# Optimization experiments

Measured on AMD Instinct MI355X. Metric: run time of the kernel, lower is better.

Reference implementation:

```python
import jax, jax.numpy as jnp
import numpy as np

NUM_HEADS = 8
NUM_LEVELS = 4
NUM_POINTS = 4


def setup_inputs() -> dict:
    key = jax.random.key(0)
    kq, kp, kv, k1, k2, k3, k4 = jax.random.split(key, 7)
    B, Q, C = 4, 4096, 256
    M, L, P = NUM_HEADS, NUM_LEVELS, NUM_POINTS
    shapes_np = np.array([[128, 128], [64, 64], [32, 32], [16, 16]], dtype=np.int32)
    sizes = shapes_np[:, 0] * shapes_np[:, 1]
    N = int(sizes.sum())  # 21760
    level_index = jnp.asarray(np.concatenate([[0], np.cumsum(sizes)[:-1]]).astype(np.int32))
    q = jax.random.normal(kq, (B, Q, C), jnp.float32)
    p = jax.random.uniform(kp, (B, Q, L, 2), jnp.float32)  # normalized ref points
    v = jax.random.normal(kv, (B, N, C), jnp.float32)
    # proj_offset bias: radial grid init from reset_parameters()
    t = np.arange(M, dtype=np.float32) * (2.0 * np.pi / M)
    grid = np.stack([np.cos(t), np.sin(t)], -1)
    grid = grid / np.abs(grid).max(-1, keepdims=True)
    grid = np.tile(grid[:, None, None, :], (1, L, P, 1)) * np.arange(1, P + 1, dtype=np.float32)[None, None, :, None]
    b_off = jnp.asarray(grid.reshape(-1))
    s = 1.0 / np.sqrt(C).astype(np.float32)
    W_off = jax.random.normal(k1, (C, M * L * P * 2), jnp.float32) * 0.01
    W_attn = jax.random.normal(k2, (C, M * L * P), jnp.float32) * s
    b_attn = jnp.zeros((M * L * P,), jnp.float32)
    W_val = jax.random.normal(k3, (C, C), jnp.float32) * s
    b_val = jnp.zeros((C,), jnp.float32)
    W_out = jax.random.normal(k4, (C, C), jnp.float32) * s
    b_out = jnp.zeros((C,), jnp.float32)
    return {"q": q, "p": p, "v": v, "shapes": jnp.asarray(shapes_np), "level_index": level_index,
            "W_off": W_off, "b_off": b_off, "W_attn": W_attn, "b_attn": b_attn,
            "W_val": W_val, "b_val": b_val, "W_out": W_out, "b_out": b_out}


def _ms_deform_attn(q, p, v, shapes, level_index, W_off, b_off, W_attn, b_attn, W_val, b_val, W_out, b_out):
    B, Q, C = q.shape
    M, L, P = NUM_HEADS, NUM_LEVELS, NUM_POINTS
    D = C // M
    N = v.shape[1]
    # value projection -> [B, M, N, D] (head-major for gather)
    v_p = (v @ W_val + b_val).reshape(B, N, M, D).transpose(0, 2, 1, 3)
    # attention weights, softmax over L*P (classic MSDeformAttn kernel contract)
    attn = jax.nn.softmax((q @ W_attn + b_attn).reshape(B, Q, M, L * P), axis=-1)
    attn = attn.reshape(B, Q, M, L, P)
    # sampling locations (P==2 reference-point branch)
    off = (q @ W_off + b_off).reshape(B, Q, M, L, P, 2)
    norm = jnp.stack([shapes[:, 1], shapes[:, 0]], -1).astype(jnp.float32)  # (W, H) per level
    loc = p[:, :, None, :, None, :] + off / norm[None, None, None, :, None, :]  # [B,Q,M,L,P,2]

    out = jnp.zeros((B, M, Q, D), jnp.float32)
    for l in range(L):
        Hf = shapes[l, 0].astype(jnp.float32)
        Wf = shapes[l, 1].astype(jnp.float32)
        Hi = shapes[l, 0]
        Wi = shapes[l, 1]
        base = level_index[l]
        # grid_sample(align_corners=False) convention: pixel = loc*size - 0.5
        x = loc[:, :, :, l, :, 0] * Wf - 0.5  # [B,Q,M,P]
        y = loc[:, :, :, l, :, 1] * Hf - 0.5
        x0 = jnp.floor(x)
        y0 = jnp.floor(y)
        lx, ly = x - x0, y - y0
        x0i = x0.astype(jnp.int32)
        y0i = y0.astype(jnp.int32)

        def corner(xi, yi, w):
            valid = (xi >= 0) & (xi < Wi) & (yi >= 0) & (yi < Hi)
            idx = base + jnp.clip(yi, 0, Hi - 1) * Wi + jnp.clip(xi, 0, Wi - 1)  # [B,Q,M,P]
            idx = idx.transpose(0, 2, 1, 3).reshape(B, M, Q * P)
            g = jnp.take_along_axis(v_p, idx[..., None], axis=2).reshape(B, M, Q, P, D)
            wv = (w * valid.astype(w.dtype)).transpose(0, 2, 1, 3)[..., None]  # [B,M,Q,P,1]
            return g * wv

        samp = (corner(x0i, y0i, (1 - lx) * (1 - ly))
                + corner(x0i + 1, y0i, lx * (1 - ly))
                + corner(x0i, y0i + 1, (1 - lx) * ly)
                + corner(x0i + 1, y0i + 1, lx * ly))  # [B,M,Q,P,D]
        a_l = attn[:, :, :, l, :].transpose(0, 2, 1, 3)  # [B,M,Q,P]
        out = out + jnp.einsum('bmqpd,bmqp->bmqd', samp, a_l)

    out = out.transpose(0, 2, 1, 3).reshape(B, Q, M * D)
    return out @ W_out + b_out


def reference(q, p, v, shapes, level_index, W_off, b_off, W_attn, b_attn, W_val, b_val, W_out, b_out):
    return _ms_deform_attn(q, p, v, shapes, level_index, W_off, b_off, W_attn, b_attn, W_val, b_val, W_out, b_out)
```

## Files before the change

### kernel.cpp

```cpp
#include <hip/hip_runtime.h>
#include <cstddef>

#define BB 4
#define QQ 4096
#define MM 8
#define NN 21760

typedef __bf16 bf16_8 __attribute__((ext_vector_type(8)));
typedef __bf16 bf16_4 __attribute__((ext_vector_type(4)));
typedef float  floatx4 __attribute__((ext_vector_type(4)));

__global__ __launch_bounds__(256) void prep_weights(
    const float* __restrict__ Wv, const float* __restrict__ Wa,
    const float* __restrict__ Wo, const float* __restrict__ Wu,
    const float* __restrict__ ba, const float* __restrict__ bo,
    __bf16* __restrict__ Wt, float* __restrict__ biasq)
{
    const int gid = blockIdx.x * 256 + threadIdx.x;
    if (gid < 65536) {
        const int n = gid >> 8, k = gid & 255;
        Wt[gid] = (__bf16)Wv[k * 256 + n];
    } else if (gid < 163840) {
        const int o = gid - 65536;
        const int n = o >> 8, k = o & 255;
        Wt[gid] = (__bf16)(n < 128 ? Wa[k * 128 + n] : Wo[k * 256 + (n - 128)]);
    } else if (gid < 229376) {
        const int o = gid - 163840;
        const int n = o >> 8, k = o & 255;
        Wt[gid] = (__bf16)Wu[k * 256 + n];
    } else if (gid < 229760) {
        const int j = gid - 229376;
        biasq[j] = (j < 128) ? ba[j] : bo[j - 128];
    }
}

__global__ __launch_bounds__(256) void gemm_qproj(
    const float* __restrict__ A,
    const __bf16* __restrict__ Bt,
    const float* __restrict__ bias,
    float* __restrict__ Cout,
    int tokens, int Ncols)
{
    const int row0 = blockIdx.y * 128;
    const int col0 = blockIdx.x * 128;

    __shared__ __bf16 As[128][40];
    __shared__ __bf16 Bs[128][40];

    const int tid  = threadIdx.x;
    const int lane = tid & 63;
    const int wave = tid >> 6;
    const int quad = lane >> 4;
    const int l16  = lane & 15;
    const int wave_m = (wave & 1) * 64;
    const int wave_n = (wave >> 1) * 64;

    floatx4 acc[4][4] = {};

    const int a_row  = tid >> 3;
    const int a_kc   = (tid & 7) * 4;
    const int b_n    = tid >> 1;
    const int b_c0   = (tid & 1) * 8;

    for (int k0 = 0; k0 < 256; k0 += 32) {
        #pragma unroll
        for (int j = 0; j < 4; ++j) {
            const int r = a_row + j * 32;
            const float4 av = *(const float4*)(A + (size_t)(row0 + r) * 256 + k0 + a_kc);
            bf16_4 bv;
            bv[0] = (__bf16)av.x; bv[1] = (__bf16)av.y;
            bv[2] = (__bf16)av.z; bv[3] = (__bf16)av.w;
            *(bf16_4*)&As[r][a_kc] = bv;
        }
        #pragma unroll
        for (int j = 0; j < 2; ++j) {
            const int kc = b_c0 + j * 16;
            *(bf16_8*)&Bs[b_n][kc] =
                *(const bf16_8*)(Bt + (size_t)(col0 + b_n) * 256 + k0 + kc);
        }
        __syncthreads();

        bf16_8 af[4], bfr[4];
        #pragma unroll
        for (int i = 0; i < 4; ++i)
            af[i] = *(const bf16_8*)&As[wave_m + i * 16 + l16][quad * 8];
        #pragma unroll
        for (int j = 0; j < 4; ++j)
            bfr[j] = *(const bf16_8*)&Bs[wave_n + j * 16 + l16][quad * 8];
        #pragma unroll
        for (int i = 0; i < 4; ++i)
            #pragma unroll
            for (int j = 0; j < 4; ++j)
                acc[i][j] = __builtin_amdgcn_mfma_f32_16x16x32_bf16(af[i], bfr[j], acc[i][j], 0, 0, 0);
        __syncthreads();
    }

    #pragma unroll
    for (int j = 0; j < 4; ++j) {
        const int col = col0 + wave_n + j * 16 + l16;
        const float bc = bias[col];
        #pragma unroll
        for (int i = 0; i < 4; ++i) {
            #pragma unroll
            for (int r = 0; r < 4; ++r) {
                const int row = row0 + wave_m + i * 16 + quad * 4 + r;
                Cout[(size_t)row * Ncols + col] = acc[i][j][r] + bc;
            }
        }
    }
}

template<typename AT, int MODE>
__global__ __launch_bounds__(256) void gemm_n256(
    const AT* __restrict__ A,
    const __bf16* __restrict__ Bt,
    const float* __restrict__ bias,
    void* __restrict__ Cout,
    int tokens)
{
    const int z    = blockIdx.z;
    const int row0 = blockIdx.y * 64;
    const AT* Ab = A + (size_t)z * tokens * 256;

    __shared__ __bf16 As[64][40];
    __shared__ __bf16 Bs[256][40];

    const int tid  = threadIdx.x;
    const int lane = tid & 63;
    const int wave = tid >> 6;
    const int quad = lane >> 4;
    const int l16  = lane & 15;
    const int wave_n = wave * 64;

    floatx4 acc[4][4] = {};

    const int a_r  = tid >> 2;
    const int a_kc = (tid & 3) * 8;
    const int b_r  = tid >> 2;
    const int b_kc = (tid & 3) * 8;

    for (int k0 = 0; k0 < 256; k0 += 32) {
        if (sizeof(AT) == 4) {
            const float* Af = (const float*)Ab;
            const float4 a0 = *(const float4*)(Af + (size_t)(row0 + a_r) * 256 + k0 + a_kc);
            const float4 a1 = *(const float4*)(Af + (size_t)(row0 + a_r) * 256 + k0 + a_kc + 4);
            bf16_8 bv;
            bv[0] = (__bf16)a0.x; bv[1] = (__bf16)a0.y; bv[2] = (__bf16)a0.z; bv[3] = (__bf16)a0.w;
            bv[4] = (__bf16)a1.x; bv[5] = (__bf16)a1.y; bv[6] = (__bf16)a1.z; bv[7] = (__bf16)a1.w;
            *(bf16_8*)&As[a_r][a_kc] = bv;
        } else {
            const __bf16* Ah = (const __bf16*)Ab;
            *(bf16_8*)&As[a_r][a_kc] =
                *(const bf16_8*)(Ah + (size_t)(row0 + a_r) * 256 + k0 + a_kc);
        }
        #pragma unroll
        for (int j = 0; j < 4; ++j) {
            const int n = b_r + j * 64;
            *(bf16_8*)&Bs[n][b_kc] =
                *(const bf16_8*)(Bt + (size_t)n * 256 + k0 + b_kc);
        }
        __syncthreads();

        bf16_8 af[4], bfr[4];
        #pragma unroll
        for (int i = 0; i < 4; ++i)
            af[i] = *(const bf16_8*)&As[i * 16 + l16][quad * 8];
        #pragma unroll
        for (int j = 0; j < 4; ++j)
            bfr[j] = *(const bf16_8*)&Bs[wave_n + j * 16 + l16][quad * 8];
        #pragma unroll
        for (int i = 0; i < 4; ++i)
            #pragma unroll
            for (int j = 0; j < 4; ++j)
                acc[i][j] = __builtin_amdgcn_mfma_f32_16x16x32_bf16(af[i], bfr[j], acc[i][j], 0, 0, 0);
        __syncthreads();
    }

    #pragma unroll
    for (int j = 0; j < 4; ++j) {
        const int col = wave_n + j * 16 + l16;
        const float bc = bias[col];
        #pragma unroll
        for (int i = 0; i < 4; ++i) {
            #pragma unroll
            for (int r = 0; r < 4; ++r) {
                const int row = row0 + i * 16 + quad * 4 + r;
                const float val = acc[i][j][r] + bc;
                if (MODE == 0) {
                    ((float*)Cout)[((size_t)z * tokens + row) * 256 + col] = val;
                } else {
                    const int m = col >> 5, dd = col & 31;
                    ((__bf16*)Cout)[(((size_t)z * 8 + m) * NN + row) * 32 + dd] = (__bf16)val;
                }
            }
        }
    }
}

__device__ __forceinline__ float bflo(unsigned u) { return __uint_as_float(u << 16); }
__device__ __forceinline__ float bfhi(unsigned u) { return __uint_as_float(u & 0xffff0000u); }

__global__ __launch_bounds__(512) void sampler(
    const __bf16* __restrict__ vp,
    const float* __restrict__ gqp,
    const float* __restrict__ pref,
    __bf16* __restrict__ mid)
{
    const int t    = threadIdx.x;
    const int m    = t >> 6;
    const int lane = t & 63;
    const int s    = lane >> 2;
    const int c    = lane & 3;
    const int l    = s >> 2;
    const int bq   = blockIdx.x;
    const int b    = bq >> 12;

    const int   Hi = 128 >> l;
    const float Hf = (float)Hi;
    const int   base = (l == 0) ? 0 : (l == 1) ? 16384 : (l == 2) ? 20480 : 21504;

    const float logit = gqp[(size_t)bq * 384 + m * 16 + s];
    const float e = __expf(logit);
    float sum = e;
    #pragma unroll
    for (int k = 4; k < 64; k <<= 1) sum += __shfl_xor(sum, k, 64);
    const float a = e * __builtin_amdgcn_rcpf(sum);

    const float2 off = *(const float2*)(gqp + (size_t)bq * 384 + 128 + (m * 16 + s) * 2);
    const float2 pr  = *(const float2*)(pref + (size_t)bq * 8 + l * 2);

    const float x = fmaf(pr.x, Hf, off.x - 0.5f);
    const float y = fmaf(pr.y, Hf, off.y - 0.5f);
    const float x0f = floorf(x), y0f = floorf(y);
    const float lx = x - x0f, ly = y - y0f;
    const int x0 = (int)x0f, y0 = (int)y0f;
    const int cx0 = min(max(x0, 0), Hi - 1), cx1 = min(max(x0 + 1, 0), Hi - 1);
    const int cy0 = min(max(y0, 0), Hi - 1), cy1 = min(max(y0 + 1, 0), Hi - 1);
    const bool vx0 = (x0 >= 0) && (x0 < Hi), vx1 = (x0 + 1 >= 0) && (x0 + 1 < Hi);
    const bool vy0 = (y0 >= 0) && (y0 < Hi), vy1 = (y0 + 1 >= 0) && (y0 + 1 < Hi);
    const float w00 = a * (1.f - lx) * (1.f - ly) * ((vx0 && vy0) ? 1.f : 0.f);
    const float w10 = a * lx * (1.f - ly) * ((vx1 && vy0) ? 1.f : 0.f);
    const float w01 = a * (1.f - lx) * ly * ((vx0 && vy1) ? 1.f : 0.f);
    const float w11 = a * lx * ly * ((vx1 && vy1) ? 1.f : 0.f);

    const __bf16* vbase = vp + ((size_t)b * 8 + m) * NN * 32;
    const uint4 u00 = *((const uint4*)(vbase + (size_t)(base + cy0 * Hi + cx0) * 32) + c);
    const uint4 u10 = *((const uint4*)(vbase + (size_t)(base + cy0 * Hi + cx1) * 32) + c);
    const uint4 u01 = *((const uint4*)(vbase + (size_t)(base + cy1 * Hi + cx0) * 32) + c);
    const uint4 u11 = *((const uint4*)(vbase + (size_t)(base + cy1 * Hi + cx1) * 32) + c);

    float f[8];
    f[0] = w00*bflo(u00.x) + w10*bflo(u10.x) + w01*bflo(u01.x) + w11*bflo(u11.x);
    f[1] = w00*bfhi(u00.x) + w10*bfhi(u10.x) + w01*bfhi(u01.x) + w11*bfhi(u11.x);
    f[2] = w00*bflo(u00.y) + w10*bflo(u10.y) + w01*bflo(u01.y) + w11*bflo(u11.y);
    f[3] = w00*bfhi(u00.y) + w10*bfhi(u10.y) + w01*bfhi(u01.y) + w11*bfhi(u11.y);
    f[4] = w00*bflo(u00.z) + w10*bflo(u10.z) + w01*bflo(u01.z) + w11*bflo(u11.z);
    f[5] = w00*bfhi(u00.z) + w10*bfhi(u10.z) + w01*bfhi(u01.z) + w11*bfhi(u11.z);
    f[6] = w00*bflo(u00.w) + w10*bflo(u10.w) + w01*bflo(u01.w) + w11*bflo(u11.w);
    f[7] = w00*bfhi(u00.w) + w10*bfhi(u10.w) + w01*bfhi(u01.w) + w11*bfhi(u11.w);

    const int b2 = (lane >> 2) & 1, b3 = (lane >> 3) & 1, b4 = (lane >> 4) & 1;
    #pragma unroll
    for (int j = 0; j < 4; ++j) {
        const float sel  = b2 ? f[j] : f[j + 4];
        const float recv = __shfl_xor(sel, 4, 64);
        f[j] = (b2 ? f[j + 4] : f[j]) + recv;
    }
    #pragma unroll
    for (int j = 0; j < 2; ++j) {
        const float sel  = b3 ? f[j] : f[j + 2];
        const float recv = __shfl_xor(sel, 8, 64);
        f[j] = (b3 ? f[j + 2] : f[j]) + recv;
    }
    {
        const float sel  = b4 ? f[0] : f[1];
        const float recv = __shfl_xor(sel, 16, 64);
        f[0] = (b4 ? f[1] : f[0]) + recv;
    }
    f[0] += __shfl_xor(f[0], 32, 64);

    if (!(lane & 32)) {
        const int chan = (c << 3) | (b2 << 2) | (b3 << 1) | b4;
        mid[(size_t)bq * 256 + m * 32 + chan] = (__bf16)f[0];
    }
}

extern "C" void kernel_launch(void* const* d_in, const int* in_sizes, int n_in,
                              void* d_out, int out_size, void* d_ws, size_t ws_size,
                              hipStream_t stream) {
    const float* q      = (const float*)d_in[0];
    const float* p      = (const float*)d_in[1];
    const float* v      = (const float*)d_in[2];
    const float* W_off  = (const float*)d_in[5];
    const float* b_off  = (const float*)d_in[6];
    const float* W_attn = (const float*)d_in[7];
    const float* b_attn = (const float*)d_in[8];
    const float* W_val  = (const float*)d_in[9];
    const float* b_val  = (const float*)d_in[10];
    const float* W_out  = (const float*)d_in[11];
    const float* b_out  = (const float*)d_in[12];
    float* out = (float*)d_out;

    float*  gqp   = (float*)d_ws;
    float*  biasq = gqp + (size_t)16384 * 384;
    __bf16* mid   = (__bf16*)(biasq + 384);
    __bf16* vpb   = mid + (size_t)16384 * 256;
    __bf16* Wt    = vpb + (size_t)BB * 8 * NN * 32;
    __bf16* Wt_val = Wt;
    __bf16* Wt_q   = Wt + 65536;
    __bf16* Wt_out = Wt + 163840;

    prep_weights<<<898, 256, 0, stream>>>(W_val, W_attn, W_off, W_out, b_attn, b_off, Wt, biasq);

    {
        dim3 grid(1, NN / 64, BB);
        gemm_n256<float, 1><<<grid, 256, 0, stream>>>(v, Wt_val, b_val, vpb, NN);
    }
    {
        dim3 grid(3, (BB * QQ) / 128, 1);
        gemm_qproj<<<grid, 256, 0, stream>>>(q, Wt_q, biasq, gqp, BB * QQ, 384);
    }
    sampler<<<BB * QQ, 512, 0, stream>>>(vpb, gqp, p, mid);
    {
        dim3 grid(1, (BB * QQ) / 64, 1);
        gemm_n256<__bf16, 0><<<grid, 256, 0, stream>>>(mid, Wt_out, b_out, out, BB * QQ);
    }
}
```

Baseline: 267.8 us.

## Unify GEMMs into K64-step template with register-staged loads and split q-projection

```diff
diff --git a/kernel.cpp b/kernel.cpp
--- a/kernel.cpp
+++ b/kernel.cpp
@@ -34,150 +34,111 @@
     }
 }
 
-__global__ __launch_bounds__(256) void gemm_qproj(
-    const float* __restrict__ A,
+template<typename AT, int NCOLS, int MODE>
+__global__ __launch_bounds__(256) void gemm_k64(
+    const AT* __restrict__ A,
     const __bf16* __restrict__ Bt,
     const float* __restrict__ bias,
-    float* __restrict__ Cout,
-    int tokens, int Ncols)
+    void* __restrict__ Cout,
+    int tokens, int ldc)
 {
-    const int row0 = blockIdx.y * 128;
-    const int col0 = blockIdx.x * 128;
-
-    __shared__ __bf16 As[128][40];
-    __shared__ __bf16 Bs[128][40];
+    constexpr int NJ  = NCOLS / 64;
+    constexpr int BCH = NCOLS / 32;
+
+    const int z    = blockIdx.z;
+    const int row0 = blockIdx.y * 64;
+    const AT* Ab = A + (size_t)z * tokens * 256;
+
+    __shared__ __bf16 As[64][68];
+    __shared__ __bf16 Bs[NCOLS][68];
 
     const int tid  = threadIdx.x;
     const int lane = tid & 63;
     const int wave = tid >> 6;
     const int quad = lane >> 4;
     const int l16  = lane & 15;
-    const int wave_m = (wave & 1) * 64;
-    const int wave_n = (wave >> 1) * 64;
-
-    floatx4 acc[4][4] = {};
-
-    const int a_row  = tid >> 3;
-    const int a_kc   = (tid & 7) * 4;
-    const int b_n    = tid >> 1;
-    const int b_c0   = (tid & 1) * 8;
-
-    for (int k0 = 0; k0 < 256; k0 += 32) {
-        #pragma unroll
-        for (int j = 0; j < 4; ++j) {
-            const int r = a_row + j * 32;
-            const float4 av = *(const float4*)(A + (size_t)(row0 + r) * 256 + k0 + a_kc);
-            bf16_4 bv;
-            bv[0] = (__bf16)av.x; bv[1] = (__bf16)av.y;
-            bv[2] = (__bf16)av.z; bv[3] = (__bf16)av.w;
-            *(bf16_4*)&As[r][a_kc] = bv;
-        }
-        #pragma unroll
-        for (int j = 0; j < 2; ++j) {
-            const int kc = b_c0 + j * 16;
-            *(bf16_8*)&Bs[b_n][kc] =
-                *(const bf16_8*)(Bt + (size_t)(col0 + b_n) * 256 + k0 + kc);
-        }
-        __syncthreads();
-
-        bf16_8 af[4], bfr[4];
-        #pragma unroll
-        for (int i = 0; i < 4; ++i)
-            af[i] = *(const bf16_8*)&As[wave_m + i * 16 + l16][quad * 8];
-        #pragma unroll
-        for (int j = 0; j < 4; ++j)
-            bfr[j] = *(const bf16_8*)&Bs[wave_n + j * 16 + l16][quad * 8];
-        #pragma unroll
-        for (int i = 0; i < 4; ++i)
-            #pragma unroll
-            for (int j = 0; j < 4; ++j)
-                acc[i][j] = __builtin_amdgcn_mfma_f32_16x16x32_bf16(af[i], bfr[j], acc[i][j], 0, 0, 0);
-        __syncthreads();
-    }
-
-    #pragma unroll
-    for (int j = 0; j < 4; ++j) {
-        const int col = col0 + wave_n + j * 16 + l16;
-        const float bc = bias[col];
-        #pragma unroll
-        for (int i = 0; i < 4; ++i) {
-            #pragma unroll
-            for (int r = 0; r < 4; ++r) {
-                const int row = row0 + wave_m + i * 16 + quad * 4 + r;
-                Cout[(size_t)row * Ncols + col] = acc[i][j][r] + bc;
-            }
-        }
-    }
-}
-
-template<typename AT, int MODE>
-__global__ __launch_bounds__(256) void gemm_n256(
-    const AT* __restrict__ A,
-    const __bf16* __restrict__ Bt,
-    const float* __restrict__ bias,
-    void* __restrict__ Cout,
-    int tokens)
-{
-    const int z    = blockIdx.z;
-    const int row0 = blockIdx.y * 64;
-    const AT* Ab = A + (size_t)z * tokens * 256;
-
-    __shared__ __bf16 As[64][40];
-    __shared__ __bf16 Bs[256][40];
-
-    const int tid  = threadIdx.x;
-    const int lane = tid & 63;
-    const int wave = tid >> 6;
-    const int quad = lane >> 4;
-    const int l16  = lane & 15;
-    const int wave_n = wave * 64;
-
-    floatx4 acc[4][4] = {};
-
-    const int a_r  = tid >> 2;
-    const int a_kc = (tid & 3) * 8;
-    const int b_r  = tid >> 2;
-    const int b_kc = (tid & 3) * 8;
-
-    for (int k0 = 0; k0 < 256; k0 += 32) {
+    const int wave_n = wave * (NCOLS / 4);
+
+    floatx4 acc[4][NJ] = {};
+
+    for (int k0 = 0; k0 < 256; k0 += 64) {
+        float4 a4[4];
+        bf16_8 a8[2];
         if (sizeof(AT) == 4) {
             const float* Af = (const float*)Ab;
-            const float4 a0 = *(const float4*)(Af + (size_t)(row0 + a_r) * 256 + k0 + a_kc);
-            const float4 a1 = *(const float4*)(Af + (size_t)(row0 + a_r) * 256 + k0 + a_kc + 4);
-            bf16_8 bv;
-            bv[0] = (__bf16)a0.x; bv[1] = (__bf16)a0.y; bv[2] = (__bf16)a0.z; bv[3] = (__bf16)a0.w;
-            bv[4] = (__bf16)a1.x; bv[5] = (__bf16)a1.y; bv[6] = (__bf16)a1.z; bv[7] = (__bf16)a1.w;
-            *(bf16_8*)&As[a_r][a_kc] = bv;
+            #pragma unroll
+            for (int c = 0; c < 4; ++c) {
+                const int cid = c * 256 + tid;
+                const int r   = cid >> 4;
+                const int kc  = (cid & 15) * 4;
+                a4[c] = *(const float4*)(Af + (size_t)(row0 + r) * 256 + k0 + kc);
+            }
         } else {
             const __bf16* Ah = (const __bf16*)Ab;
-            *(bf16_8*)&As[a_r][a_kc] =
-                *(const bf16_8*)(Ah + (size_t)(row0 + a_r) * 256 + k0 + a_kc);
-        }
-        #pragma unroll
-        for (int j = 0; j < 4; ++j) {
-            const int n = b_r + j * 64;
-            *(bf16_8*)&Bs[n][b_kc] =
-                *(const bf16_8*)(Bt + (size_t)n * 256 + k0 + b_kc);
+            #pragma unroll
+            for (int c = 0; c < 2; ++c) {
+                const int cid = c * 256 + tid;
+                const int r   = cid >> 3;
+                const int kc  = (cid & 7) * 8;
+                a8[c] = *(const bf16_8*)(Ah + (size_t)(row0 + r) * 256 + k0 + kc);
+            }
+        }
+        bf16_8 b8[BCH];
+        #pragma unroll
+        for (int c = 0; c < BCH; ++c) {
+            const int cid = c * 256 + tid;
+            const int n   = cid >> 3;
+            const int kc  = (cid & 7) * 8;
+            b8[c] = *(const bf16_8*)(Bt + (size_t)n * 256 + k0 + kc);
+        }
+        if (sizeof(AT) == 4) {
+            #pragma unroll
+            for (int c = 0; c < 4; ++c) {
+                const int cid = c * 256 + tid;
+                const int r   = cid >> 4;
+                const int kc  = (cid & 15) * 4;
+                bf16_4 w;
+                w[0] = (__bf16)a4[c].x; w[1] = (__bf16)a4[c].y;
+                w[2] = (__bf16)a4[c].z; w[3] = (__bf16)a4[c].w;
+                *(bf16_4*)&As[r][kc] = w;
+            }
+        } else {
+            #pragma unroll
+            for (int c = 0; c < 2; ++c) {
+                const int cid = c * 256 + tid;
+                const int r   = cid >> 3;
+                const int kc  = (cid & 7) * 8;
+                *(bf16_8*)&As[r][kc] = a8[c];
+            }
+        }
+        #pragma unroll
+        for (int c = 0; c < BCH; ++c) {
+            const int cid = c * 256 + tid;
+            const int n   = cid >> 3;
+            const int kc  = (cid & 7) * 8;
+            *(bf16_8*)&Bs[n][kc] = b8[c];
         }
         __syncthreads();
-
-        bf16_8 af[4], bfr[4];
-        #pragma unroll
-        for (int i = 0; i < 4; ++i)
-            af[i] = *(const bf16_8*)&As[i * 16 + l16][quad * 8];
-        #pragma unroll
-        for (int j = 0; j < 4; ++j)
-            bfr[j] = *(const bf16_8*)&Bs[wave_n + j * 16 + l16][quad * 8];
-        #pragma unroll
-        for (int i = 0; i < 4; ++i)
-            #pragma unroll
-            for (int j = 0; j < 4; ++j)
-                acc[i][j] = __builtin_amdgcn_mfma_f32_16x16x32_bf16(af[i], bfr[j], acc[i][j], 0, 0, 0);
+        #pragma unroll
+        for (int h = 0; h < 2; ++h) {
+            bf16_8 af[4], bfr[NJ];
+            #pragma unroll
+            for (int i = 0; i < 4; ++i)
+                af[i] = *(const bf16_8*)&As[i * 16 + l16][h * 32 + quad * 8];
+            #pragma unroll
+            for (int j = 0; j < NJ; ++j)
+                bfr[j] = *(const bf16_8*)&Bs[wave_n + j * 16 + l16][h * 32 + quad * 8];
+            #pragma unroll
+            for (int i = 0; i < 4; ++i)
+                #pragma unroll
+                for (int j = 0; j < NJ; ++j)
+                    acc[i][j] = __builtin_amdgcn_mfma_f32_16x16x32_bf16(af[i], bfr[j], acc[i][j], 0, 0, 0);
+        }
         __syncthreads();
     }
 
     #pragma unroll
-    for (int j = 0; j < 4; ++j) {
+    for (int j = 0; j < NJ; ++j) {
         const int col = wave_n + j * 16 + l16;
         const float bc = bias[col];
         #pragma unroll
@@ -187,7 +148,7 @@
                 const int row = row0 + i * 16 + quad * 4 + r;
                 const float val = acc[i][j][r] + bc;
                 if (MODE == 0) {
-                    ((float*)Cout)[((size_t)z * tokens + row) * 256 + col] = val;
+                    ((float*)Cout)[((size_t)z * tokens + row) * ldc + col] = val;
                 } else {
                     const int m = col >> 5, dd = col & 31;
                     ((__bf16*)Cout)[(((size_t)z * 8 + m) * NN + row) * 32 + dd] = (__bf16)val;
@@ -306,23 +267,28 @@
     __bf16* mid   = (__bf16*)(biasq + 384);
     __bf16* vpb   = mid + (size_t)16384 * 256;
     __bf16* Wt    = vpb + (size_t)BB * 8 * NN * 32;
-    __bf16* Wt_val = Wt;
-    __bf16* Wt_q   = Wt + 65536;
-    __bf16* Wt_out = Wt + 163840;
+    __bf16* Wt_val  = Wt;
+    __bf16* Wt_attn = Wt + 65536;
+    __bf16* Wt_off  = Wt + 65536 + 32768;
+    __bf16* Wt_out  = Wt + 163840;
 
     prep_weights<<<898, 256, 0, stream>>>(W_val, W_attn, W_off, W_out, b_attn, b_off, Wt, biasq);
 
     {
         dim3 grid(1, NN / 64, BB);
-        gemm_n256<float, 1><<<grid, 256, 0, stream>>>(v, Wt_val, b_val, vpb, NN);
-    }
-    {
-        dim3 grid(3, (BB * QQ) / 128, 1);
-        gemm_qproj<<<grid, 256, 0, stream>>>(q, Wt_q, biasq, gqp, BB * QQ, 384);
+        gemm_k64<float, 256, 1><<<grid, 256, 0, stream>>>(v, Wt_val, b_val, vpb, NN, 0);
+    }
+    {
+        dim3 grid(1, (BB * QQ) / 64, 1);
+        gemm_k64<float, 128, 0><<<grid, 256, 0, stream>>>(q, Wt_attn, biasq, gqp, BB * QQ, 384);
+    }
+    {
+        dim3 grid(1, (BB * QQ) / 64, 1);
+        gemm_k64<float, 256, 0><<<grid, 256, 0, stream>>>(q, Wt_off, biasq + 128, gqp + 128, BB * QQ, 384);
     }
     sampler<<<BB * QQ, 512, 0, stream>>>(vpb, gqp, p, mid);
     {
         dim3 grid(1, (BB * QQ) / 64, 1);
-        gemm_n256<__bf16, 0><<<grid, 256, 0, stream>>>(mid, Wt_out, b_out, out, BB * QQ);
-    }
-}
+        gemm_k64<__bf16, 256, 0><<<grid, 256, 0, stream>>>(mid, Wt_out, b_out, out, BB * QQ, 256);
+    }
+}
```

New measurement: 258.1 us. 3.6% less time.
